# Performance work log

Measured on AMD Instinct MI355X. Metric: run time of the kernel, lower is better.

The kernel has to match this reference:

```python
import jax, jax.numpy as jnp
import numpy as np

B, N_C, N_F = 2, 16384, 65536          # batch, coarse nodes, fine (up_nodes)
C_IN, C_OUT = 128, 128
E_C, E_F = 65536, 262144               # coarse / fine edge counts


def _mlp_params(key, cin, cout):
    # 2-layer MLP (Linear-ReLU-Linear) + LayerNorm, torch default uniform init
    k1, k2 = jax.random.split(key)
    s1 = 1.0 / np.sqrt(2 * cin)
    s2 = 1.0 / np.sqrt(cout)
    W1 = jax.random.uniform(k1, (2 * cin, cout), minval=-s1, maxval=s1, dtype=jnp.float32)
    W2 = jax.random.uniform(k2, (cout, cout), minval=-s2, maxval=s2, dtype=jnp.float32)
    return (W1, jnp.zeros((cout,), jnp.float32), W2, jnp.zeros((cout,), jnp.float32),
            jnp.ones((cout,), jnp.float32), jnp.zeros((cout,), jnp.float32))


def setup_inputs() -> dict:
    key = jax.random.key(0)
    rng = np.random.default_rng(0)
    x = jax.random.normal(jax.random.fold_in(key, 1), (B, N_C, C_IN), dtype=jnp.float32)
    # sorted unique unpool indices (m_id)
    idx = jnp.asarray(np.sort(rng.choice(N_F, N_C, replace=False)).astype(np.int64))
    ei_c = jnp.asarray(rng.integers(0, N_C, size=(2, E_C)).astype(np.int64))
    ei_f = jnp.asarray(rng.integers(0, N_F, size=(2, E_F)).astype(np.int64))
    d = {"x": x, "idx": idx, "ei_c": ei_c, "ei_f": ei_f}
    for pre, k, cin, cout in (("s", 2, C_IN, C_OUT), ("a", 3, C_IN, C_OUT // 2), ("b", 4, C_OUT // 2, C_OUT)):
        W1, b1, W2, b2, g, bt = _mlp_params(jax.random.fold_in(key, k), cin, cout)
        d.update({pre + "W1": W1, pre + "b1": b1, pre + "W2": W2, pre + "b2": b2, pre + "g": g, pre + "bt": bt})
    return d


def _unpool(x, idx, n):
    # scatter coarse features into a zero-filled fine array (Unpool module)
    return jnp.zeros((x.shape[0], n, x.shape[-1]), x.dtype).at[:, idx].set(x)


def _edgeconv(x, ei, W1, b1, W2, b2, g, bt, n):
    # EdgeConv: aggregate_sum over edges of MLP([x_i, x_j - x_i]) + LayerNorm
    src, dst = ei[0], ei[1]
    xd = x[:, dst]                                   # [B,E,cin] gather at target
    feat = jnp.concatenate([xd, x[:, src] - xd], axis=-1)  # [B,E,2*cin]
    h = jax.nn.relu(feat @ W1 + b1) @ W2 + b2        # [B,E,cout]
    mu = jnp.mean(h, axis=-1, keepdims=True)
    var = jnp.var(h, axis=-1, keepdims=True)
    h = (h - mu) * jax.lax.rsqrt(var + 1e-5) * g + bt
    return jax.vmap(lambda hb: jax.ops.segment_sum(hb, dst, num_segments=n))(h)


def reference(x, idx, ei_c, ei_f,
              sW1, sb1, sW2, sb2, sg, sbt,
              aW1, ab1, aW2, ab2, ag, abt,
              bW1, bb1, bW2, bb2, bg, bbt):
    # skip branch: unpool then EdgeConv cin->cout on fine graph
    skip = _edgeconv(_unpool(x, idx, N_F), ei_f, sW1, sb1, sW2, sb2, sg, sbt, N_F)
    # main branch: EdgeConv cin->cout/2 on coarse, unpool, EdgeConv cout/2->cout on fine
    h = _edgeconv(x, ei_c, aW1, ab1, aW2, ab2, ag, abt, N_C)
    h = _edgeconv(_unpool(h, idx, N_F), ei_f, bW1, bb1, bW2, bb2, bg, bbt, N_F)
    return jax.nn.leaky_relu(h + skip, 0.01)
```

## Files before the change

### kernel.cpp

```cpp
#include <hip/hip_runtime.h>

typedef _Float16 half8  __attribute__((ext_vector_type(8)));
typedef _Float16 half4v __attribute__((ext_vector_type(4)));
typedef _Float16 half2v __attribute__((ext_vector_type(2)));
typedef float    f32x4  __attribute__((ext_vector_type(4)));
typedef float    f32x2  __attribute__((ext_vector_type(2)));
typedef int      i32x4  __attribute__((ext_vector_type(4)));

#define NB 2
#define N_C 16384
#define N_F 65536
#define E_C 65536
#define E_F 262144

#define INV4  ((size_t)N_F / 4)
#define CNT4  ((size_t)(N_F + N_C) / 4)

__global__ void clear_small(int* __restrict__ inv, int* __restrict__ cnt) {
    size_t i = (size_t)blockIdx.x * 256 + threadIdx.x;
    const i32x4 z = {0, 0, 0, 0};
    const i32x4 m1 = {-1, -1, -1, -1};
    if (i < INV4) ((i32x4*)inv)[i] = m1;
    else if (i < INV4 + CNT4) ((i32x4*)cnt)[i - INV4] = z;
}

__device__ inline void swizzle_dev(const float* __restrict__ W, _Float16* __restrict__ Ws,
                                   int N, int o) {
    int j = o & 7;
    int lane = (o >> 3) & 63;
    int frag = o >> 9;
    int ntiles = N >> 4;
    int nt = frag % ntiles;
    int kt = frag / ntiles;
    int k = kt * 32 + (lane >> 4) * 8 + j;
    int n = nt * 16 + (lane & 15);
    Ws[o] = (_Float16)W[k * N + n];
}

__device__ inline void swz_node(const float* __restrict__ W, _Float16* __restrict__ Ws,
                                int CIN, int COUT, int o) {
    int j = o & 7;
    int lane = (o >> 3) & 63;
    int frag = o >> 9;
    int N2 = 2 * COUT;
    int ntiles = N2 >> 4;
    int nt = frag % ntiles;
    int kt = frag / ntiles;
    int k = kt * 32 + (lane >> 4) * 8 + j;
    int n = nt * 16 + (lane & 15);
    float v = (n < COUT) ? W[k * COUT + n] - W[(k + CIN) * COUT + n]
                         : W[(k + CIN) * COUT + (n - COUT)];
    Ws[o] = (_Float16)v;
}

__global__ void setup_all(const int* __restrict__ idx, int* __restrict__ inv,
                          const float* sW1, const float* sW2, const float* aW1,
                          const float* aW2, const float* bW1, const float* bW2,
                          const float* sb1, const float* ab1, const float* bb1,
                          _Float16* sW1n, _Float16* sW2s, _Float16* aW1n,
                          _Float16* aW2s, _Float16* bW1n, _Float16* bW2s,
                          _Float16* b1h,
                          const int* __restrict__ ei_f, const int* __restrict__ ei_c,
                          int* __restrict__ cnt) {
    const int bb = blockIdx.x, t = threadIdx.x;
    if (bb < 64) {
        int i = bb * 256 + t;
        inv[idx[i]] = i;
    } else if (bb < 192) {
        swz_node(sW1, sW1n, 128, 128, (bb - 64) * 256 + t);
    } else if (bb < 256) {
        swizzle_dev(sW2, sW2s, 128, (bb - 192) * 256 + t);
    } else if (bb < 320) {
        swz_node(aW1, aW1n, 128, 64, (bb - 256) * 256 + t);
    } else if (bb < 336) {
        swizzle_dev(aW2, aW2s, 64, (bb - 320) * 256 + t);
    } else if (bb < 400) {
        swz_node(bW1, bW1n, 64, 128, (bb - 336) * 256 + t);
    } else if (bb < 464) {
        swizzle_dev(bW2, bW2s, 128, (bb - 400) * 256 + t);
    } else if (bb < 466) {
        int i = (bb - 464) * 256 + t;
        if (i < 128) b1h[i] = (_Float16)sb1[i];
        else if (i < 192) b1h[i] = (_Float16)ab1[i - 128];
        else if (i < 320) b1h[i] = (_Float16)bb1[i - 192];
    } else if (bb < 1490) {
        int e = (bb - 466) * 256 + t;
        atomicAdd(&cnt[ei_f[E_F + e]], 1);
    } else {
        int e = (bb - 1490) * 256 + t;
        atomicAdd(&cnt[N_F + ei_c[E_C + e]], 1);
    }
}

__global__ void scan1(const int* __restrict__ cnt, int* __restrict__ csum) {
    __shared__ int red[4];
    int v = cnt[blockIdx.x * 256 + threadIdx.x];
    #pragma unroll
    for (int off = 32; off >= 1; off >>= 1) v += __shfl_xor(v, off, 64);
    if ((threadIdx.x & 63) == 0) red[threadIdx.x >> 6] = v;
    __syncthreads();
    if (threadIdx.x == 0) csum[blockIdx.x] = red[0] + red[1] + red[2] + red[3];
}

__global__ void scan3zf(const int* __restrict__ cnt, const int* __restrict__ csum,
                        int* __restrict__ cursor, unsigned char* __restrict__ flagF,
                        float* __restrict__ out, float* __restrict__ h_a) {
    __shared__ int buf[256];
    __shared__ int red[4];
    const int t = threadIdx.x, bb = blockIdx.x;

    const int lo = (bb < 256) ? 0 : 256;
    int part = 0;
    for (int j = lo + t; j < bb; j += 256) part += csum[j];
    #pragma unroll
    for (int off = 32; off >= 1; off >>= 1) part += __shfl_xor(part, off, 64);
    if ((t & 63) == 0) red[t >> 6] = part;

    const int d = bb * 256 + t;
    int v = cnt[d];
    buf[t] = v;
    __syncthreads();
    const int base = red[0] + red[1] + red[2] + red[3];
    for (int off = 1; off < 256; off <<= 1) {
        int u = (t >= off) ? buf[t - off] : 0;
        __syncthreads();
        buf[t] += u;
        __syncthreads();
    }
    const int start = base + buf[t] - v;
    cursor[d] = start;
    const int deg = v;
    const int end = start + deg;
    const f32x4 z = {0.f, 0.f, 0.f, 0.f};
    if (d < N_F) {
        const bool pred = (deg == 0) || ((start >> 5) != ((end - 1) >> 5));
        flagF[d] = pred ? 1 : 0;
        if (pred) {
            f32x4* r0 = (f32x4*)(out + (size_t)d * 128);
            f32x4* r1 = (f32x4*)(out + ((size_t)N_F + d) * 128);
            #pragma unroll
            for (int i = 0; i < 32; ++i) { r0[i] = z; r1[i] = z; }
        }
    } else {
        const int dc = d - N_F;
        const bool pred = (deg == 0) || ((start >> 4) != ((end - 1) >> 4));
        if (pred) {
            f32x4* r0 = (f32x4*)(h_a + (size_t)dc * 64);
            f32x4* r1 = (f32x4*)(h_a + ((size_t)N_C + dc) * 64);
            #pragma unroll
            for (int i = 0; i < 16; ++i) { r0[i] = z; r1[i] = z; }
        }
    }
}

template <int CIN, int COUT>
__device__ void node_gemm_body(const float* __restrict__ x, const _Float16* __restrict__ W1n,
                               const float* __restrict__ b1, _Float16* __restrict__ P,
                               _Float16* L, int blk, int t) {
    constexpr int N2 = 2 * COUT;
    constexpr int FP = CIN + 8;
    constexpr int P2 = N2 + 8;
    constexpr int NPW = N2 / 4;
    constexpr int NT = NPW / 16;

    const size_t r0 = (size_t)blk * 64;

    {
        const int m = t >> 2, l4 = t & 3;
        const float* src = x + (r0 + m) * CIN + l4 * (CIN / 4);
        #pragma unroll
        for (int i = 0; i < CIN / 16; ++i) {
            f32x4 v = *(const f32x4*)(src + i * 4);
            half4v h;
            #pragma unroll
            for (int c = 0; c < 4; ++c) h[c] = (_Float16)v[c];
            *(half4v*)(L + m * FP + l4 * (CIN / 4) + i * 4) = h;
        }
    }
    __syncthreads();

    const int wv = t >> 6, lane = t & 63;
    const int q = lane >> 4, lm = lane & 15;
    const int n0 = wv * NPW;
    const f32x4 zero4 = {0.f, 0.f, 0.f, 0.f};

    f32x4 acc[4][NT];
    #pragma unroll
    for (int mt = 0; mt < 4; ++mt)
        #pragma unroll
        for (int nt = 0; nt < NT; ++nt) acc[mt][nt] = zero4;

    __builtin_amdgcn_s_setprio(1);
    #pragma unroll
    for (int kt = 0; kt < CIN / 32; ++kt) {
        half8 a[4];
        #pragma unroll
        for (int mt = 0; mt < 4; ++mt)
            a[mt] = *(const half8*)(L + (mt * 16 + lm) * FP + kt * 32 + q * 8);
        #pragma unroll
        for (int nt = 0; nt < NT; ++nt) {
            half8 bf = *(const half8*)(W1n + ((size_t)(kt * (N2 / 16) + wv * NT + nt) * 64 + lane) * 8);
            #pragma unroll
            for (int mt = 0; mt < 4; ++mt)
                acc[mt][nt] = __builtin_amdgcn_mfma_f32_16x16x32_f16(a[mt], bf, acc[mt][nt], 0, 0, 0);
        }
    }
    __builtin_amdgcn_s_setprio(0);
    __syncthreads();

    #pragma unroll
    for (int nt = 0; nt < NT; ++nt) {
        const int col = n0 + nt * 16 + lm;
        const float bv = (col < COUT) ? b1[col] : 0.f;
        #pragma unroll
        for (int mt = 0; mt < 4; ++mt)
            #pragma unroll
            for (int r = 0; r < 4; ++r)
                L[(mt * 16 + q * 4 + r) * P2 + col] = (_Float16)(acc[mt][nt][r] + bv);
    }
    __syncthreads();

    constexpr int CH = 64 * N2 / 8;
    for (int i = t; i < CH; i += 256) {
        int row = i / (N2 / 8), c8 = i % (N2 / 8);
        *(half8*)(P + (r0 + row) * N2 + c8 * 8) = *(const half8*)(L + row * P2 + c8 * 8);
    }
}

__launch_bounds__(256, 4) __global__
void scatter_nodesa(const int* __restrict__ ei_f, const int* __restrict__ ei_c,
                    const int* __restrict__ inv, int* __restrict__ cursor,
                    i32x4* __restrict__ ef_info, i32x4* __restrict__ ec_info,
                    const float* __restrict__ x,
                    const _Float16* __restrict__ sW1n, const float* __restrict__ sb1,
                    _Float16* __restrict__ Ps,
                    const _Float16* __restrict__ aW1n, const float* __restrict__ ab1,
                    _Float16* __restrict__ Pa) {
    __shared__ __align__(16) _Float16 L[16896];
    const int bb = blockIdx.x, t = threadIdx.x;
    if (bb < 1024) {
        int e = bb * 256 + t;
        int s_ = ei_f[e];
        int d_ = ei_f[E_F + e];
        int p = atomicAdd(&cursor[d_], 1);
        i32x4 rec;
        rec.x = inv[s_]; rec.y = inv[d_]; rec.z = d_; rec.w = 0;
        ef_info[p] = rec;
    } else if (bb < 1280) {
        int e = (bb - 1024) * 256 + t;
        int s_ = ei_c[e];
        int d_ = ei_c[E_C + e];
        int p = atomicAdd(&cursor[N_F + d_], 1);
        i32x4 rec;
        rec.x = s_; rec.y = d_; rec.z = d_; rec.w = 0;
        ec_info[p] = rec;
    } else if (bb < 1280 + NB * N_C / 64) {
        node_gemm_body<128, 128>(x, sW1n, sb1, Ps, L, bb - 1280, t);
    } else {
        node_gemm_body<128, 64>(x, aW1n, ab1, Pa, L, bb - 1280 - NB * N_C / 64, t);
    }
}

template <int CIN, int COUT>
__launch_bounds__(256, 4) __global__
void node_gemm(const float* __restrict__ x, const _Float16* __restrict__ W1n,
               const float* __restrict__ b1, _Float16* __restrict__ P) {
    __shared__ __align__(16) _Float16 L[16896];
    node_gemm_body<CIN, COUT>(x, W1n, b1, P, L, blockIdx.x, threadIdx.x);
}

__device__ inline half8 relu8(half8 h) {
#if __has_builtin(__builtin_elementwise_max)
    half8 z = {};
    return __builtin_elementwise_max(h, z);
#else
    #pragma unroll
    for (int i = 0; i < 8; ++i) h[i] = h[i] > (_Float16)0 ? h[i] : (_Float16)0;
    return h;
#endif
}

template <int COUT, bool FRESH>
__launch_bounds__(256, 8) __global__
void edge2_mfma(const _Float16* __restrict__ P, int ps,
                const i32x4* __restrict__ einfo, int E,
                const _Float16* __restrict__ W2s, const float* __restrict__ b2,
                const float* __restrict__ g, const float* __restrict__ bt,
                const _Float16* __restrict__ b1h,
                float* __restrict__ dest, int bs_out) {
    constexpr int HPITCH = COUT + 8;
    constexpr int NPW = COUT / 4;
    constexpr int NT = NPW / 16;

    __shared__ __align__(16) _Float16 region[64 * HPITCH];
    __shared__ int dstl[64];
    __shared__ int dpnL[2];
    __shared__ float muL[64];
    __shared__ float rsL[64];

    _Float16* h1L = region;
    _Float16* vnL = region;

    const int t = threadIdx.x;
    const int eb = blockIdx.x * 64;
    const int b = eb / E;
    const int e0 = eb - b * E;

    {
        if (t == 0) dpnL[0] = (e0 > 0) ? einfo[e0 - 1].z : -2;
        else if (t == 1) dpnL[1] = (e0 + 64 < E) ? einfo[e0 + 64].z : -2;
        const int m = t >> 2, l4 = t & 3;
        const i32x4 rec = einfo[e0 + m];
        const int si = rec.x, di = rec.y;
        if (l4 == 0) dstl[m] = rec.z;
        const _Float16* pb = P + (size_t)b * ps;
        const _Float16* ub = (di >= 0) ? pb + (size_t)di * (2 * COUT) : b1h;
        const _Float16* vb = pb + (size_t)(si >= 0 ? si : 0) * (2 * COUT) + COUT;
        constexpr int CPT = COUT / 4;
        const int c0 = l4 * CPT;
        #pragma unroll
        for (int i = 0; i < CPT / 8; ++i) {
            half8 u = *(const half8*)(ub + c0 + i * 8);
            half8 v = {};
            if (si >= 0) v = *(const half8*)(vb + c0 + i * 8);
            *(half8*)(h1L + m * HPITCH + c0 + i * 8) = relu8(u + v);
        }
    }
    __syncthreads();

    const int wv = t >> 6, lane = t & 63;
    const int q = lane >> 4, lm = lane & 15;
    const int n0 = wv * NPW;
    const f32x4 zero4 = {0.f, 0.f, 0.f, 0.f};

    f32x4 acc[4][NT];
    #pragma unroll
    for (int mt = 0; mt < 4; ++mt)
        #pragma unroll
        for (int nt = 0; nt < NT; ++nt) acc[mt][nt] = zero4;

    __builtin_amdgcn_s_setprio(1);
    #pragma unroll
    for (int kt = 0; kt < COUT / 32; ++kt) {
        half8 a[4];
        #pragma unroll
        for (int mt = 0; mt < 4; ++mt)
            a[mt] = *(const half8*)(h1L + (mt * 16 + lm) * HPITCH + kt * 32 + q * 8);
        #pragma unroll
        for (int nt = 0; nt < NT; ++nt) {
            half8 bf = *(const half8*)(W2s + ((size_t)(kt * (COUT / 16) + wv * NT + nt) * 64 + lane) * 8);
            #pragma unroll
            for (int mt = 0; mt < 4; ++mt)
                acc[mt][nt] = __builtin_amdgcn_mfma_f32_16x16x32_f16(a[mt], bf, acc[mt][nt], 0, 0, 0);
        }
    }
    __builtin_amdgcn_s_setprio(0);
    __syncthreads();

    #pragma unroll
    for (int nt = 0; nt < NT; ++nt) {
        const float b2v = b2[n0 + nt * 16 + lm];
        #pragma unroll
        for (int mt = 0; mt < 4; ++mt)
            #pragma unroll
            for (int r = 0; r < 4; ++r)
                vnL[(mt * 16 + q * 4 + r) * HPITCH + n0 + nt * 16 + lm] =
                    (_Float16)(acc[mt][nt][r] + b2v);
    }
    __syncthreads();

    {
        const int m = t >> 2, p = t & 3;
        constexpr int CPT = COUT / 4;
        float s = 0.f, s2 = 0.f;
        #pragma unroll
        for (int c = 0; c < CPT / 8; ++c) {
            half8 h8 = *(const half8*)(vnL + m * HPITCH + p * CPT + c * 8);
            #pragma unroll
            for (int j = 0; j < 8; ++j) {
                float v = (float)h8[j];
                s += v;
                s2 += v * v;
            }
        }
        s += __shfl_xor(s, 1, 64);  s2 += __shfl_xor(s2, 1, 64);
        s += __shfl_xor(s, 2, 64);  s2 += __shfl_xor(s2, 2, 64);
        if (p == 0) {
            float mu = s * (1.f / COUT);
            muL[m] = mu;
            rsL[m] = rsqrtf(s2 * (1.f / COUT) - mu * mu + 1e-5f);
        }
    }
    __syncthreads();

    {
        constexpr int CG = COUT / 64;
        constexpr int W  = 4 / CG;
        constexpr int RW = 64 / W;
        const int wv2 = t >> 6, l2 = t & 63;
        const int cg = wv2 % CG;
        const int h  = wv2 / CG;
        const int c  = cg * 64 + l2;
        const int r0 = h * RW;
        const float gv = g[c], bv = bt[c];
        float* const ob = dest + (size_t)b * bs_out + c;
        int dcur = dstl[r0];
        const int dprev = (r0 == 0) ? dpnL[0] : dstl[r0 - 1];
        bool bflag = (dcur == dprev);
        float rs = 0.f;
        #pragma unroll
        for (int i = 0; i < RW; ++i) {
            const int m = r0 + i;
            const float v = (float)vnL[m * HPITCH + c];
            rs += (v - muL[m]) * rsL[m] * gv + bv;
            const int dnxt = (i == RW - 1)
                               ? ((r0 + RW == 64) ? dpnL[1] : dstl[r0 + RW])
                               : dstl[m + 1];
            if (dnxt != dcur) {
                if (!FRESH || bflag) atomicAdd(ob + (size_t)dcur * COUT, rs);
                else ob[(size_t)dcur * COUT] = rs;
                rs = 0.f; dcur = dnxt; bflag = false;
            } else if (i == RW - 1) {
                atomicAdd(ob + (size_t)dcur * COUT, rs);
            }
        }
    }
}

__launch_bounds__(256, 4) __global__
void edge2_dual(const _Float16* __restrict__ Ps, const _Float16* __restrict__ Pb,
                const i32x4* __restrict__ einfo,
                const _Float16* __restrict__ W2sS, const float* __restrict__ b2s,
                const float* __restrict__ gS, const float* __restrict__ btS,
                const _Float16* __restrict__ W2sB, const float* __restrict__ b2b,
                const float* __restrict__ gB, const float* __restrict__ btB,
                const _Float16* __restrict__ b1hS, const _Float16* __restrict__ b1hB,
                float* __restrict__ out) {
    constexpr int E = E_F;
    constexpr int HP = 136;
    constexpr int IP = 264;

    __shared__ __align__(16) _Float16 region[2 * 64 * HP];
    __shared__ int dstl[64];
    __shared__ int dpn[2];
    __shared__ f32x4 stat4[64];

    _Float16* h1S = region;
    _Float16* h1B = region + 64 * HP;
    _Float16* vnI = region;

    const int t = threadIdx.x;
    const int eb = blockIdx.x * 64;
    const int b = eb / E;
    const int e0 = eb - b * E;

    {
        if (t == 0) dpn[0] = (e0 > 0) ? einfo[e0 - 1].z : -2;
        else if (t == 1) dpn[1] = (e0 + 64 < E) ? einfo[e0 + 64].z : -2;
        const int m = t >> 2, l4 = t & 3;
        const i32x4 rec = einfo[e0 + m];
        const int si = rec.x, di = rec.y;
        if (l4 == 0) dstl[m] = rec.z;
        const size_t pofs = (size_t)b * ((size_t)N_C * 256);
        const _Float16* ubS = (di >= 0) ? Ps + pofs + (size_t)di * 256 : b1hS;
        const _Float16* ubB = (di >= 0) ? Pb + pofs + (size_t)di * 256 : b1hB;
        const size_t so = (size_t)(si >= 0 ? si : 0) * 256 + 128;
        const _Float16* vbS = Ps + pofs + so;
        const _Float16* vbB = Pb + pofs + so;
        const int c0 = l4 * 32;
        #pragma unroll
        for (int i = 0; i < 4; ++i) {
            half8 uS = *(const half8*)(ubS + c0 + i * 8);
            half8 uB = *(const half8*)(ubB + c0 + i * 8);
            half8 vS = {}, vB = {};
            if (si >= 0) {
                vS = *(const half8*)(vbS + c0 + i * 8);
                vB = *(const half8*)(vbB + c0 + i * 8);
            }
            *(half8*)(h1S + m * HP + c0 + i * 8) = relu8(uS + vS);
            *(half8*)(h1B + m * HP + c0 + i * 8) = relu8(uB + vB);
        }
    }
    __syncthreads();

    const int wv = t >> 6, lane = t & 63;
    const int q = lane >> 4, lm = lane & 15;
    const int n0 = wv * 32;
    const f32x4 zero4 = {0.f, 0.f, 0.f, 0.f};

    f32x4 accS[4][2], accB[4][2];
    #pragma unroll
    for (int mt = 0; mt < 4; ++mt)
        #pragma unroll
        for (int nt = 0; nt < 2; ++nt) { accS[mt][nt] = zero4; accB[mt][nt] = zero4; }

    __builtin_amdgcn_s_setprio(1);
    #pragma unroll
    for (int kt = 0; kt < 4; ++kt) {
        half8 aS[4], aB[4];
        #pragma unroll
        for (int mt = 0; mt < 4; ++mt) {
            aS[mt] = *(const half8*)(h1S + (mt * 16 + lm) * HP + kt * 32 + q * 8);
            aB[mt] = *(const half8*)(h1B + (mt * 16 + lm) * HP + kt * 32 + q * 8);
        }
        #pragma unroll
        for (int nt = 0; nt < 2; ++nt) {
            half8 bS = *(const half8*)(W2sS + ((size_t)(kt * 8 + wv * 2 + nt) * 64 + lane) * 8);
            half8 bB = *(const half8*)(W2sB + ((size_t)(kt * 8 + wv * 2 + nt) * 64 + lane) * 8);
            #pragma unroll
            for (int mt = 0; mt < 4; ++mt) {
                accS[mt][nt] = __builtin_amdgcn_mfma_f32_16x16x32_f16(aS[mt], bS, accS[mt][nt], 0, 0, 0);
                accB[mt][nt] = __builtin_amdgcn_mfma_f32_16x16x32_f16(aB[mt], bB, accB[mt][nt], 0, 0, 0);
            }
        }
    }
    __builtin_amdgcn_s_setprio(0);
    __syncthreads();

    #pragma unroll
    for (int nt = 0; nt < 2; ++nt) {
        const int col = n0 + nt * 16 + lm;
        const float b2vS = b2s[col];
        const float b2vB = b2b[col];
        #pragma unroll
        for (int mt = 0; mt < 4; ++mt)
            #pragma unroll
            for (int r = 0; r < 4; ++r) {
                const int row = mt * 16 + q * 4 + r;
                half2v pk;
                pk[0] = (_Float16)(accS[mt][nt][r] + b2vS);
                pk[1] = (_Float16)(accB[mt][nt][r] + b2vB);
                *(half2v*)(vnI + row * IP + col * 2) = pk;
            }
    }
    __syncthreads();

    {
        const int m = t >> 2, p = t & 3;
        float sS = 0.f, s2S = 0.f, sB = 0.f, s2B = 0.f;
        #pragma unroll
        for (int k = 0; k < 8; ++k) {
            half8 h8 = *(const half8*)(vnI + m * IP + p * 64 + k * 8);
            #pragma unroll
            for (int j = 0; j < 8; j += 2) {
                float a = (float)h8[j];     sS += a; s2S += a * a;
                float c = (float)h8[j + 1]; sB += c; s2B += c * c;
            }
        }
        sS += __shfl_xor(sS, 1, 64);  s2S += __shfl_xor(s2S, 1, 64);
        sS += __shfl_xor(sS, 2, 64);  s2S += __shfl_xor(s2S, 2, 64);
        sB += __shfl_xor(sB, 1, 64);  s2B += __shfl_xor(s2B, 1, 64);
        sB += __shfl_xor(sB, 2, 64);  s2B += __shfl_xor(s2B, 2, 64);
        if (p == 0) {
            const float mS = sS * (1.f / 128.f);
            const float rS = rsqrtf(s2S * (1.f / 128.f) - mS * mS + 1e-5f);
            const float mB = sB * (1.f / 128.f);
            const float rB = rsqrtf(s2B * (1.f / 128.f) - mB * mB + 1e-5f);
            f32x4 st;
            st[0] = rS; st[1] = -mS * rS; st[2] = rB; st[3] = -mB * rB;
            stat4[m] = st;
        }
    }
    __syncthreads();

    {
        const int wv2 = t >> 6, l2 = t & 63;
        const int cg = wv2 & 1;
        const int h  = wv2 >> 1;
        const int c  = cg * 64 + l2;
        const int r0 = h * 32;
        const float gS_ = gS[c], gB_ = gB[c];
        const float bsum = btS[c] + btB[c];
        float* const ob = out + (size_t)b * ((size_t)N_F * 128) + c;
        int dcur = dstl[r0];
        const int dprev = (r0 == 0) ? dpn[0] : dstl[r0 - 1];
        bool bflag = (dcur == dprev);
        float rs = 0.f;
        #pragma unroll
        for (int i = 0; i < 32; ++i) {
            const int m = r0 + i;
            const half2v v2 = *(const half2v*)(vnI + m * IP + c * 2);
            const f32x4 st = stat4[m];
            rs += fmaf((float)v2[0], st[0], st[1]) * gS_
                + fmaf((float)v2[1], st[2], st[3]) * gB_ + bsum;
            const int dnxt = (i == 31)
                               ? ((r0 + 32 == 64) ? dpn[1] : dstl[r0 + 32])
                               : dstl[m + 1];
            if (dnxt != dcur) {
                if (bflag) {
                    atomicAdd(ob + (size_t)dcur * 128, rs);
                } else {
                    float v = rs > 0.f ? rs : 0.01f * rs;
                    ob[(size_t)dcur * 128] = v;
                }
                rs = 0.f; dcur = dnxt; bflag = false;
            } else if (i == 31) {
                atomicAdd(ob + (size_t)dcur * 128, rs);
            }
        }
    }
}

__global__ void leaky_fix(float* __restrict__ out, const unsigned char* __restrict__ flagF) {
    const size_t i = (size_t)blockIdx.x * 256 + threadIdx.x;
    if (i >= (size_t)NB * N_F * 32) return;
    const int d = (int)((i >> 5) & (N_F - 1));
    if (!flagF[d]) return;
    f32x4 v = ((f32x4*)out)[i];
    #pragma unroll
    for (int c = 0; c < 4; ++c) v[c] = v[c] > 0.f ? v[c] : 0.01f * v[c];
    ((f32x4*)out)[i] = v;
}

extern "C" void kernel_launch(void* const* d_in, const int* in_sizes, int n_in,
                              void* d_out, int out_size, void* d_ws, size_t ws_size,
                              hipStream_t stream) {
    const float* x    = (const float*)d_in[0];
    const int*   idx  = (const int*)d_in[1];
    const int*   ei_c = (const int*)d_in[2];
    const int*   ei_f = (const int*)d_in[3];
    const float* sW1 = (const float*)d_in[4];
    const float* sb1 = (const float*)d_in[5];
    const float* sW2 = (const float*)d_in[6];
    const float* sb2 = (const float*)d_in[7];
    const float* sg  = (const float*)d_in[8];
    const float* sbt = (const float*)d_in[9];
    const float* aW1 = (const float*)d_in[10];
    const float* ab1 = (const float*)d_in[11];
    const float* aW2 = (const float*)d_in[12];
    const float* ab2 = (const float*)d_in[13];
    const float* ag  = (const float*)d_in[14];
    const float* abt = (const float*)d_in[15];
    const float* bW1 = (const float*)d_in[16];
    const float* bb1 = (const float*)d_in[17];
    const float* bW2 = (const float*)d_in[18];
    const float* bb2 = (const float*)d_in[19];
    const float* bg  = (const float*)d_in[20];
    const float* bbt = (const float*)d_in[21];

    float* out = (float*)d_out;

    char* ws = (char*)d_ws;
    int*   inv    = (int*)ws;                                ws += (size_t)N_F * 4;
    float* h_a    = (float*)ws;                              ws += (size_t)NB * N_C * 64 * 4;
    int*   cnt    = (int*)ws;                                ws += (size_t)(N_F + N_C) * 4;
    int*   cursor = (int*)ws;                                ws += (size_t)(N_F + N_C) * 4;
    int*   csum   = (int*)ws;                                ws += 320 * 4;
    int*   cbase  = (int*)ws;                                ws += 320 * 4;
    i32x4* ef_info = (i32x4*)ws;                             ws += (size_t)E_F * 16;
    i32x4* ec_info = (i32x4*)ws;                             ws += (size_t)E_C * 16;
    _Float16* sW1n = (_Float16*)ws;                          ws += (size_t)128 * 256 * 2;
    _Float16* sW2s = (_Float16*)ws;                          ws += (size_t)128 * 128 * 2;
    _Float16* aW1n = (_Float16*)ws;                          ws += (size_t)128 * 128 * 2;
    _Float16* aW2s = (_Float16*)ws;                          ws += (size_t)64 * 64 * 2;
    _Float16* bW1n = (_Float16*)ws;                          ws += (size_t)64 * 256 * 2;
    _Float16* bW2s = (_Float16*)ws;                          ws += (size_t)128 * 128 * 2;
    _Float16* b1h  = (_Float16*)ws;                          ws += 1024;
    unsigned char* flagF = (unsigned char*)ws;               ws += (size_t)N_F;
    _Float16* P_s  = (_Float16*)ws;                          ws += (size_t)NB * N_C * 256 * 2;
    _Float16* P_a  = (_Float16*)ws;                          ws += (size_t)NB * N_C * 128 * 2;
    _Float16* P_b  = (_Float16*)ws;                          ws += (size_t)NB * N_C * 256 * 2;
    (void)cbase;

    clear_small<<<(int)((INV4 + CNT4 + 255) / 256), 256, 0, stream>>>(inv, cnt);

    setup_all<<<1746, 256, 0, stream>>>(idx, inv, sW1, sW2, aW1, aW2, bW1, bW2,
                                        sb1, ab1, bb1,
                                        sW1n, sW2s, aW1n, aW2s, bW1n, bW2s, b1h,
                                        ei_f, ei_c, cnt);

    scan1<<<320, 256, 0, stream>>>(cnt, csum);

    scan3zf<<<320, 256, 0, stream>>>(cnt, csum, cursor, flagF, out, h_a);

    scatter_nodesa<<<1280 + 2 * (NB * N_C / 64), 256, 0, stream>>>(
        ei_f, ei_c, inv, cursor, ef_info, ec_info,
        x, sW1n, sb1, P_s, aW1n, ab1, P_a);

    edge2_mfma<64, true><<<NB * E_C / 64, 256, 0, stream>>>(
        P_a, N_C * 128, ec_info, E_C, aW2s, ab2, ag, abt, b1h + 128, h_a, N_C * 64);

    node_gemm<64, 128><<<NB * N_C / 64, 256, 0, stream>>>(h_a, bW1n, bb1, P_b);

    edge2_dual<<<NB * E_F / 64, 256, 0, stream>>>(
        P_s, P_b, ef_info,
        sW2s, sb2, sg, sbt,
        bW2s, bb2, bg, bbt,
        b1h, b1h + 192, out);

    leaky_fix<<<(int)(((size_t)NB * N_F * 32 + 255) / 256), 256, 0, stream>>>(out, flagF);
}
```

Before: 274.6 us.

## Process two 64-edge tiles per block in edge2_dual with prefetched gathers

edge2_dual now handles 128 edges per block as two sequential 64-edge tiles, halving the grid. The second tile's source-row gathers are issued into registers before the first tile's MFMA/LayerNorm/scatter and consumed afterwards, so global latency overlaps compute. __syncthreads is replaced by a custom lgkmcnt-wait plus s_barrier with a sched_barrier. The extra prefetch registers may lower occupancy, and the hand-made barrier relies on LDS-only ordering.

```diff
diff --git a/kernel.cpp b/kernel.cpp
--- a/kernel.cpp
+++ b/kernel.cpp
@@ -15,6 +15,12 @@
 
 #define INV4  ((size_t)N_F / 4)
 #define CNT4  ((size_t)(N_F + N_C) / 4)
+
+__device__ __forceinline__ void lds_barrier() {
+    asm volatile("s_waitcnt lgkmcnt(0)" ::: "memory");
+    __builtin_amdgcn_s_barrier();
+    __builtin_amdgcn_sched_barrier(0);
+}
 
 __global__ void clear_small(int* __restrict__ inv, int* __restrict__ cnt) {
     size_t i = (size_t)blockIdx.x * 256 + threadIdx.x;
@@ -441,164 +447,202 @@
     constexpr int IP = 264;
 
     __shared__ __align__(16) _Float16 region[2 * 64 * HP];
-    __shared__ int dstl[64];
-    __shared__ int dpn[2];
+    __shared__ int dstl[128];
+    __shared__ int dpnE[2];
     __shared__ f32x4 stat4[64];
 
-    _Float16* h1S = region;
-    _Float16* h1B = region + 64 * HP;
-    _Float16* vnI = region;
+    _Float16* const h1S = region;
+    _Float16* const h1B = region + 64 * HP;
+    _Float16* const vnI = region;
 
     const int t = threadIdx.x;
-    const int eb = blockIdx.x * 64;
+    const int eb = blockIdx.x * 128;
     const int b = eb / E;
     const int e0 = eb - b * E;
 
+    const int gm = t >> 2, gl4 = t & 3;
+    const int gc0 = gl4 * 32;
+    const size_t pofs = (size_t)b * ((size_t)N_C * 256);
+
+    const int wv = t >> 6, lane = t & 63;
+    const int q = lane >> 4, lm = lane & 15;
+    const int n0 = wv * 32;
+
+    auto run_tile = [&](int dOff, int dPrev, int dNext) {
+        const f32x4 zero4 = {0.f, 0.f, 0.f, 0.f};
+        f32x4 accS[4][2], accB[4][2];
+        #pragma unroll
+        for (int mt = 0; mt < 4; ++mt)
+            #pragma unroll
+            for (int nt = 0; nt < 2; ++nt) { accS[mt][nt] = zero4; accB[mt][nt] = zero4; }
+
+        __builtin_amdgcn_s_setprio(1);
+        #pragma unroll
+        for (int kt = 0; kt < 4; ++kt) {
+            half8 aS[4], aB[4];
+            #pragma unroll
+            for (int mt = 0; mt < 4; ++mt) {
+                aS[mt] = *(const half8*)(h1S + (mt * 16 + lm) * HP + kt * 32 + q * 8);
+                aB[mt] = *(const half8*)(h1B + (mt * 16 + lm) * HP + kt * 32 + q * 8);
+            }
+            #pragma unroll
+            for (int nt = 0; nt < 2; ++nt) {
+                half8 bS = *(const half8*)(W2sS + ((size_t)(kt * 8 + wv * 2 + nt) * 64 + lane) * 8);
+                half8 bB = *(const half8*)(W2sB + ((size_t)(kt * 8 + wv * 2 + nt) * 64 + lane) * 8);
+                #pragma unroll
+                for (int mt = 0; mt < 4; ++mt) {
+                    accS[mt][nt] = __builtin_amdgcn_mfma_f32_16x16x32_f16(aS[mt], bS, accS[mt][nt], 0, 0, 0);
+                    accB[mt][nt] = __builtin_amdgcn_mfma_f32_16x16x32_f16(aB[mt], bB, accB[mt][nt], 0, 0, 0);
+                }
+            }
+        }
+        __builtin_amdgcn_s_setprio(0);
+        lds_barrier();
+
+        #pragma unroll
+        for (int nt = 0; nt < 2; ++nt) {
+            const int col = n0 + nt * 16 + lm;
+            const float b2vS = b2s[col];
+            const float b2vB = b2b[col];
+            #pragma unroll
+            for (int mt = 0; mt < 4; ++mt)
+                #pragma unroll
+                for (int r = 0; r < 4; ++r) {
+                    const int row = mt * 16 + q * 4 + r;
+                    half2v pk;
+                    pk[0] = (_Float16)(accS[mt][nt][r] + b2vS);
+                    pk[1] = (_Float16)(accB[mt][nt][r] + b2vB);
+                    *(half2v*)(vnI + row * IP + col * 2) = pk;
+                }
+        }
+        lds_barrier();
+
+        {
+            const int m = t >> 2, p = t & 3;
+            float sS = 0.f, s2S = 0.f, sB = 0.f, s2B = 0.f;
+            #pragma unroll
+            for (int k = 0; k < 8; ++k) {
+                half8 h8 = *(const half8*)(vnI + m * IP + p * 64 + k * 8);
+                #pragma unroll
+                for (int j = 0; j < 8; j += 2) {
+                    float a = (float)h8[j];     sS += a; s2S += a * a;
+                    float c = (float)h8[j + 1]; sB += c; s2B += c * c;
+                }
+            }
+            sS += __shfl_xor(sS, 1, 64);  s2S += __shfl_xor(s2S, 1, 64);
+            sS += __shfl_xor(sS, 2, 64);  s2S += __shfl_xor(s2S, 2, 64);
+            sB += __shfl_xor(sB, 1, 64);  s2B += __shfl_xor(s2B, 1, 64);
+            sB += __shfl_xor(sB, 2, 64);  s2B += __shfl_xor(s2B, 2, 64);
+            if (p == 0) {
+                const float mS = sS * (1.f / 128.f);
+                const float rS = rsqrtf(s2S * (1.f / 128.f) - mS * mS + 1e-5f);
+                const float mB = sB * (1.f / 128.f);
+                const float rB = rsqrtf(s2B * (1.f / 128.f) - mB * mB + 1e-5f);
+                f32x4 st;
+                st[0] = rS; st[1] = -mS * rS; st[2] = rB; st[3] = -mB * rB;
+                stat4[m] = st;
+            }
+        }
+        lds_barrier();
+
+        {
+            const int wv2 = t >> 6, l2 = t & 63;
+            const int cg = wv2 & 1;
+            const int h  = wv2 >> 1;
+            const int c  = cg * 64 + l2;
+            const int r0 = h * 32;
+            const float gS_ = gS[c], gB_ = gB[c];
+            const float bsum = btS[c] + btB[c];
+            float* const ob = out + (size_t)b * ((size_t)N_F * 128) + c;
+            int dcur = dstl[dOff + r0];
+            const int dprev = (r0 == 0) ? dPrev : dstl[dOff + r0 - 1];
+            bool bflag = (dcur == dprev);
+            float rs = 0.f;
+            #pragma unroll
+            for (int i = 0; i < 32; ++i) {
+                const int m = r0 + i;
+                const half2v v2 = *(const half2v*)(vnI + m * IP + c * 2);
+                const f32x4 st = stat4[m];
+                rs += fmaf((float)v2[0], st[0], st[1]) * gS_
+                    + fmaf((float)v2[1], st[2], st[3]) * gB_ + bsum;
+                const int dnxt = (i == 31)
+                                   ? ((r0 + 32 == 64) ? dNext : dstl[dOff + r0 + 32])
+                                   : dstl[dOff + m + 1];
+                if (dnxt != dcur) {
+                    if (bflag) {
+                        atomicAdd(ob + (size_t)dcur * 128, rs);
+                    } else {
+                        float v = rs > 0.f ? rs : 0.01f * rs;
+                        ob[(size_t)dcur * 128] = v;
+                    }
+                    rs = 0.f; dcur = dnxt; bflag = false;
+                } else if (i == 31) {
+                    atomicAdd(ob + (size_t)dcur * 128, rs);
+                }
+            }
+        }
+    };
+
+    half8 pvS[4], pvB[4];
+    int si1, di1;
     {
-        if (t == 0) dpn[0] = (e0 > 0) ? einfo[e0 - 1].z : -2;
-        else if (t == 1) dpn[1] = (e0 + 64 < E) ? einfo[e0 + 64].z : -2;
-        const int m = t >> 2, l4 = t & 3;
-        const i32x4 rec = einfo[e0 + m];
-        const int si = rec.x, di = rec.y;
-        if (l4 == 0) dstl[m] = rec.z;
-        const size_t pofs = (size_t)b * ((size_t)N_C * 256);
+        if (t == 0) dpnE[0] = (e0 > 0) ? einfo[e0 - 1].z : -2;
+        else if (t == 1) dpnE[1] = (e0 + 128 < E) ? einfo[e0 + 128].z : -2;
+        const i32x4 rec0 = einfo[e0 + gm];
+        const i32x4 rec1 = einfo[e0 + 64 + gm];
+        si1 = rec1.x; di1 = rec1.y;
+        if (gl4 == 0) { dstl[gm] = rec0.z; dstl[64 + gm] = rec1.z; }
+        const int si = rec0.x, di = rec0.y;
         const _Float16* ubS = (di >= 0) ? Ps + pofs + (size_t)di * 256 : b1hS;
         const _Float16* ubB = (di >= 0) ? Pb + pofs + (size_t)di * 256 : b1hB;
         const size_t so = (size_t)(si >= 0 ? si : 0) * 256 + 128;
         const _Float16* vbS = Ps + pofs + so;
         const _Float16* vbB = Pb + pofs + so;
-        const int c0 = l4 * 32;
         #pragma unroll
         for (int i = 0; i < 4; ++i) {
-            half8 uS = *(const half8*)(ubS + c0 + i * 8);
-            half8 uB = *(const half8*)(ubB + c0 + i * 8);
+            half8 uS = *(const half8*)(ubS + gc0 + i * 8);
+            half8 uB = *(const half8*)(ubB + gc0 + i * 8);
             half8 vS = {}, vB = {};
             if (si >= 0) {
-                vS = *(const half8*)(vbS + c0 + i * 8);
-                vB = *(const half8*)(vbB + c0 + i * 8);
+                vS = *(const half8*)(vbS + gc0 + i * 8);
+                vB = *(const half8*)(vbB + gc0 + i * 8);
             }
-            *(half8*)(h1S + m * HP + c0 + i * 8) = relu8(uS + vS);
-            *(half8*)(h1B + m * HP + c0 + i * 8) = relu8(uB + vB);
-        }
-    }
-    __syncthreads();
-
-    const int wv = t >> 6, lane = t & 63;
-    const int q = lane >> 4, lm = lane & 15;
-    const int n0 = wv * 32;
-    const f32x4 zero4 = {0.f, 0.f, 0.f, 0.f};
-
-    f32x4 accS[4][2], accB[4][2];
-    #pragma unroll
-    for (int mt = 0; mt < 4; ++mt)
-        #pragma unroll
-        for (int nt = 0; nt < 2; ++nt) { accS[mt][nt] = zero4; accB[mt][nt] = zero4; }
-
-    __builtin_amdgcn_s_setprio(1);
-    #pragma unroll
-    for (int kt = 0; kt < 4; ++kt) {
-        half8 aS[4], aB[4];
-        #pragma unroll
-        for (int mt = 0; mt < 4; ++mt) {
-            aS[mt] = *(const half8*)(h1S + (mt * 16 + lm) * HP + kt * 32 + q * 8);
-            aB[mt] = *(const half8*)(h1B + (mt * 16 + lm) * HP + kt * 32 + q * 8);
-        }
-        #pragma unroll
-        for (int nt = 0; nt < 2; ++nt) {
-            half8 bS = *(const half8*)(W2sS + ((size_t)(kt * 8 + wv * 2 + nt) * 64 + lane) * 8);
-            half8 bB = *(const half8*)(W2sB + ((size_t)(kt * 8 + wv * 2 + nt) * 64 + lane) * 8);
-            #pragma unroll
-            for (int mt = 0; mt < 4; ++mt) {
-                accS[mt][nt] = __builtin_amdgcn_mfma_f32_16x16x32_f16(aS[mt], bS, accS[mt][nt], 0, 0, 0);
-                accB[mt][nt] = __builtin_amdgcn_mfma_f32_16x16x32_f16(aB[mt], bB, accB[mt][nt], 0, 0, 0);
-            }
-        }
-    }
-    __builtin_amdgcn_s_setprio(0);
-    __syncthreads();
-
-    #pragma unroll
-    for (int nt = 0; nt < 2; ++nt) {
-        const int col = n0 + nt * 16 + lm;
-        const float b2vS = b2s[col];
-        const float b2vB = b2b[col];
-        #pragma unroll
-        for (int mt = 0; mt < 4; ++mt)
-            #pragma unroll
-            for (int r = 0; r < 4; ++r) {
-                const int row = mt * 16 + q * 4 + r;
-                half2v pk;
-                pk[0] = (_Float16)(accS[mt][nt][r] + b2vS);
-                pk[1] = (_Float16)(accB[mt][nt][r] + b2vB);
-                *(half2v*)(vnI + row * IP + col * 2) = pk;
-            }
-    }
-    __syncthreads();
+            *(half8*)(h1S + gm * HP + gc0 + i * 8) = relu8(uS + vS);
+            *(half8*)(h1B + gm * HP + gc0 + i * 8) = relu8(uB + vB);
+        }
+        const size_t so1 = (size_t)(si1 >= 0 ? si1 : 0) * 256 + 128;
+        const _Float16* vbS1 = Ps + pofs + so1;
+        const _Float16* vbB1 = Pb + pofs + so1;
+        #pragma unroll
+        for (int i = 0; i < 4; ++i) {
+            pvS[i] = *(const half8*)(vbS1 + gc0 + i * 8);
+            pvB[i] = *(const half8*)(vbB1 + gc0 + i * 8);
+        }
+    }
+    lds_barrier();
+
+    const int dNext0 = dstl[64];
+    const int dPrev1 = dstl[63];
+    run_tile(0, dpnE[0], dNext0);
+
+    lds_barrier();
 
     {
-        const int m = t >> 2, p = t & 3;
-        float sS = 0.f, s2S = 0.f, sB = 0.f, s2B = 0.f;
-        #pragma unroll
-        for (int k = 0; k < 8; ++k) {
-            half8 h8 = *(const half8*)(vnI + m * IP + p * 64 + k * 8);
-            #pragma unroll
-            for (int j = 0; j < 8; j += 2) {
-                float a = (float)h8[j];     sS += a; s2S += a * a;
-                float c = (float)h8[j + 1]; sB += c; s2B += c * c;
-            }
-        }
-        sS += __shfl_xor(sS, 1, 64);  s2S += __shfl_xor(s2S, 1, 64);
-        sS += __shfl_xor(sS, 2, 64);  s2S += __shfl_xor(s2S, 2, 64);
-        sB += __shfl_xor(sB, 1, 64);  s2B += __shfl_xor(s2B, 1, 64);
-        sB += __shfl_xor(sB, 2, 64);  s2B += __shfl_xor(s2B, 2, 64);
-        if (p == 0) {
-            const float mS = sS * (1.f / 128.f);
-            const float rS = rsqrtf(s2S * (1.f / 128.f) - mS * mS + 1e-5f);
-            const float mB = sB * (1.f / 128.f);
-            const float rB = rsqrtf(s2B * (1.f / 128.f) - mB * mB + 1e-5f);
-            f32x4 st;
-            st[0] = rS; st[1] = -mS * rS; st[2] = rB; st[3] = -mB * rB;
-            stat4[m] = st;
-        }
-    }
-    __syncthreads();
-
-    {
-        const int wv2 = t >> 6, l2 = t & 63;
-        const int cg = wv2 & 1;
-        const int h  = wv2 >> 1;
-        const int c  = cg * 64 + l2;
-        const int r0 = h * 32;
-        const float gS_ = gS[c], gB_ = gB[c];
-        const float bsum = btS[c] + btB[c];
-        float* const ob = out + (size_t)b * ((size_t)N_F * 128) + c;
-        int dcur = dstl[r0];
-        const int dprev = (r0 == 0) ? dpn[0] : dstl[r0 - 1];
-        bool bflag = (dcur == dprev);
-        float rs = 0.f;
-        #pragma unroll
-        for (int i = 0; i < 32; ++i) {
-            const int m = r0 + i;
-            const half2v v2 = *(const half2v*)(vnI + m * IP + c * 2);
-            const f32x4 st = stat4[m];
-            rs += fmaf((float)v2[0], st[0], st[1]) * gS_
-                + fmaf((float)v2[1], st[2], st[3]) * gB_ + bsum;
-            const int dnxt = (i == 31)
-                               ? ((r0 + 32 == 64) ? dpn[1] : dstl[r0 + 32])
-                               : dstl[m + 1];
-            if (dnxt != dcur) {
-                if (bflag) {
-                    atomicAdd(ob + (size_t)dcur * 128, rs);
-                } else {
-                    float v = rs > 0.f ? rs : 0.01f * rs;
-                    ob[(size_t)dcur * 128] = v;
-                }
-                rs = 0.f; dcur = dnxt; bflag = false;
-            } else if (i == 31) {
-                atomicAdd(ob + (size_t)dcur * 128, rs);
-            }
-        }
-    }
+        const _Float16* ubS = (di1 >= 0) ? Ps + pofs + (size_t)di1 * 256 : b1hS;
+        const _Float16* ubB = (di1 >= 0) ? Pb + pofs + (size_t)di1 * 256 : b1hB;
+        #pragma unroll
+        for (int i = 0; i < 4; ++i) {
+            half8 uS = *(const half8*)(ubS + gc0 + i * 8);
+            half8 uB = *(const half8*)(ubB + gc0 + i * 8);
+            half8 vS = {}, vB = {};
+            if (si1 >= 0) { vS = pvS[i]; vB = pvB[i]; }
+            *(half8*)(h1S + gm * HP + gc0 + i * 8) = relu8(uS + vS);
+            *(half8*)(h1B + gm * HP + gc0 + i * 8) = relu8(uB + vB);
+        }
+    }
+    lds_barrier();
+
+    run_tile(64, dPrev1, dpnE[1]);
 }
 
 __global__ void leaky_fix(float* __restrict__ out, const unsigned char* __restrict__ flagF) {
@@ -682,7 +726,7 @@
 
     node_gemm<64, 128><<<NB * N_C / 64, 256, 0, stream>>>(h_a, bW1n, bb1, P_b);
 
-    edge2_dual<<<NB * E_F / 64, 256, 0, stream>>>(
+    edge2_dual<<<NB * E_F / 128, 256, 0, stream>>>(
         P_s, P_b, ef_info,
         sW2s, sb2, sg, sbt,
         bW2s, bb2, bg, bbt,
```

New measurement: 381.4 us. 38.9% more time.
